# Kernel optimization log

Hardware: AMD Instinct MI355X
Metric: run time of the kernel (lower is better)

Reference implementation:

```python
import jax, jax.numpy as jnp
import numpy as np

P = 0.7
WALKS_PER_NODE = 1
WALK_LENGTH = 3


def setup_inputs() -> dict:
    key = jax.random.key(0)
    N = 1_000_000
    E = 16_000_000
    k1, k2 = jax.random.split(key)
    row = jax.random.randint(k1, (E,), 0, N)
    col = jax.random.randint(k2, (E,), 0, N)
    edge_index = jnp.stack([row, col])  # [2, E]
    return {"edge_index": edge_index, "num_nodes": N}


def reference(edge_index, num_nodes):
    E = edge_index.shape[1]
    row, col = edge_index[0], edge_index[1]

    # sort_edge_index: lexicographic sort by (row, col) via two stable argsorts
    p1 = jnp.argsort(col, stable=True)
    p2 = jnp.argsort(row[p1], stable=True)
    perm = p1[p2]
    row, col = row[perm], col[perm]

    # CSR rowptr from out-degree
    deg = jax.ops.segment_sum(jnp.ones(E, jnp.int32), row, num_segments=num_nodes)
    rowptr = jnp.concatenate([jnp.zeros(1, deg.dtype), jnp.cumsum(deg)])

    # start nodes: random permutation, take round(N*p), repeat walks_per_node times
    num_start = int(round(num_nodes * P))
    kperm, kwalk = jax.random.split(jax.random.key(42))
    start = jax.random.permutation(kperm, num_nodes)[:num_start]
    start = jnp.tile(start, WALKS_PER_NODE)  # [S]

    def step(carry, k):
        cur, active = carry
        d = deg[cur]                                  # [S] degree of current node
        act = active & (d > 0)                        # walkers with neighbors
        u = jax.random.uniform(k, cur.shape)
        off = jnp.floor(u * d.astype(u.dtype)).astype(cur.dtype)
        off = jnp.minimum(off, jnp.maximum(d - 1, 0).astype(cur.dtype))
        nxt = col[rowptr[cur] + off]                  # random neighbor gather
        # NOTE: faithful to source, e_id records current_node (used as an
        # index into the edge mask, as the original code does)
        eid = cur
        cur = jnp.where(act, nxt, cur)
        return (cur, act), (eid, act)

    keys = jax.random.split(kwalk, WALK_LENGTH)
    init = (start, jnp.ones(start.shape, bool))
    _, (e_ids, valids) = jax.lax.scan(step, init, keys)

    e_flat = e_ids.reshape(-1)
    v_flat = valids.reshape(-1)
    # scatter hits; invalid entries routed out-of-bounds and dropped
    hits = jnp.zeros(E, bool).at[jnp.where(v_flat, e_flat, E)].set(True, mode='drop')
    edge_mask = ~hits

    # fixed-shape compaction of edge_index[:, edge_mask] / edge_index[:, ~edge_mask]
    ei = jnp.stack([row, col])                        # sorted edge_index [2, E]
    order_keep = jnp.argsort(~edge_mask, stable=True)
    order_mask = jnp.argsort(edge_mask, stable=True)
    n_keep = edge_mask.sum()
    ar = jnp.arange(E)
    remaining_edges = jnp.where(ar < n_keep, ei[:, order_keep], -1)
    masked_edges = jnp.where(ar < (E - n_keep), ei[:, order_mask], -1)
    return remaining_edges, masked_edges, edge_mask
```

## Files before the change

### kernel.cpp

```cpp
#include <hip/hip_runtime.h>
#include <stdint.h>

#define THREADS 256
#define ITEMS 16
#define CHUNK (THREADS * ITEMS)
#define COLMASK 0xFFFFFu
#define EDIG 4096
#define BR 256
#define BCAP 4608
#define PDIG 1024

__host__ __device__ static inline void tf2x32(uint32_t k0, uint32_t k1,
                                              uint32_t x0, uint32_t x1,
                                              uint32_t* o0, uint32_t* o1) {
  uint32_t ks[3] = {k0, k1, k0 ^ k1 ^ 0x1BD11BDAu};
  x0 += ks[0]; x1 += ks[1];
  const uint32_t RA[4] = {13u, 15u, 26u, 6u};
  const uint32_t RB[4] = {17u, 29u, 16u, 24u};
#pragma unroll
  for (int g = 0; g < 5; ++g) {
    const uint32_t* R = (g & 1) ? RB : RA;
#pragma unroll
    for (int j = 0; j < 4; ++j) {
      x0 += x1;
      x1 = (x1 << R[j]) | (x1 >> (32u - R[j]));
      x1 ^= x0;
    }
    x0 += ks[(g + 1) % 3];
    x1 += ks[(g + 2) % 3] + (uint32_t)(g + 1);
  }
  *o0 = x0; *o1 = x1;
}

__device__ static inline uint32_t rbits32(uint32_t ka, uint32_t kb, uint32_t i) {
  uint32_t o0, o1;
  tf2x32(ka, kb, 0u, i, &o0, &o1);
  return o0 ^ o1;
}

__device__ static inline int xcd_swz(int orig, int nwg) {
  int q = nwg >> 3, r = nwg & 7;
  int xcd = orig & 7, idx = orig >> 3;
  return (xcd < r ? xcd * (q + 1) : r * (q + 1) + (xcd - r) * q) + idx;
}

__device__ static inline uint32_t block_scan_excl(uint32_t v, uint32_t* lds) {
  int t = threadIdx.x;
  lds[t] = v;
  __syncthreads();
#pragma unroll
  for (int d = 1; d < THREADS; d <<= 1) {
    uint32_t add = (t >= d) ? lds[t - d] : 0u;
    __syncthreads();
    lds[t] += add;
    __syncthreads();
  }
  return lds[t] - v;
}

__global__ void k_sums_u32(const uint32_t* __restrict__ d, int n, uint32_t* __restrict__ bsums) {
  __shared__ uint32_t lds[THREADS];
  int b = blockIdx.x, t = threadIdx.x;
  int base = b * CHUNK + t * ITEMS;
  uint32_t s = 0;
#pragma unroll
  for (int j = 0; j < ITEMS; ++j) { int i = base + j; if (i < n) s += d[i]; }
  lds[t] = s; __syncthreads();
  for (int d2 = THREADS / 2; d2 > 0; d2 >>= 1) { if (t < d2) lds[t] += lds[t + d2]; __syncthreads(); }
  if (t == 0) bsums[b] = lds[0];
}

__global__ void k_scan_single(uint32_t* __restrict__ d, int n, uint32_t* __restrict__ total_out) {
  __shared__ uint32_t lds[THREADS];
  int t = threadIdx.x;
  int K = (n + THREADS - 1) / THREADS;
  int s0 = t * K, s1 = (s0 + K < n) ? (s0 + K) : n;
  uint32_t s = 0;
  for (int j = s0; j < s1; ++j) s += d[j];
  lds[t] = s; __syncthreads();
#pragma unroll
  for (int dd = 1; dd < THREADS; dd <<= 1) {
    uint32_t a = (t >= dd) ? lds[t - dd] : 0u;
    __syncthreads();
    lds[t] += a;
    __syncthreads();
  }
  uint32_t incl = lds[t];
  if (total_out && t == THREADS - 1) *total_out = incl;
  uint32_t run = incl - s;
  for (int j = s0; j < s1; ++j) { uint32_t tmp = d[j]; d[j] = run; run += tmp; }
}

__global__ void k_excl_u32(uint32_t* __restrict__ d, int n, const uint32_t* __restrict__ bsums) {
  __shared__ uint32_t lds[THREADS];
  int b = blockIdx.x, t = threadIdx.x;
  int base = b * CHUNK + t * ITEMS;
  uint32_t v[ITEMS]; uint32_t s = 0;
#pragma unroll
  for (int j = 0; j < ITEMS; ++j) { int i = base + j; uint32_t x = (i < n) ? d[i] : 0u; v[j] = x; s += x; }
  uint32_t run = bsums[b] + block_scan_excl(s, lds);
#pragma unroll
  for (int j = 0; j < ITEMS; ++j) { int i = base + j; if (i < n) d[i] = run; run += v[j]; }
}

__global__ void k_dig_starts(const uint32_t* __restrict__ hist, int NB, int DIG, int total,
                             uint32_t* __restrict__ dstart) {
  int d = blockIdx.x * blockDim.x + threadIdx.x;
  if (d < DIG) dstart[d] = hist[(size_t)d * NB];
  else if (d == DIG) dstart[DIG] = (uint32_t)total;
}

__global__ void k_hist12(const int* __restrict__ row, int n, int NB, uint32_t* __restrict__ hist) {
  __shared__ uint32_t h[EDIG];
  int b = xcd_swz(blockIdx.x, gridDim.x), t = threadIdx.x;
#pragma unroll
  for (int g = 0; g < EDIG / THREADS; ++g) h[g * THREADS + t] = 0;
  __syncthreads();
  int base = b * CHUNK;
  for (int j = t; j < CHUNK; j += THREADS) {
    int i = base + j;
    if (i < n) atomicAdd(&h[((uint32_t)row[i]) >> 8], 1u);
  }
  __syncthreads();
#pragma unroll
  for (int g = 0; g < EDIG / THREADS; ++g) {
    int d = g * THREADS + t;
    hist[(size_t)d * NB + b] = h[d];
  }
}

__global__ __launch_bounds__(THREADS) void k_pack_scatter12(
    const int* __restrict__ row, const int* __restrict__ col,
    uint64_t* __restrict__ kout, const uint32_t* __restrict__ hist, int n, int NB) {
  constexpr int G = EDIG / THREADS;
  __shared__ uint64_t lkeys[CHUNK];
  __shared__ uint32_t cur[EDIG];
  int b = xcd_swz(blockIdx.x, gridDim.x), t = threadIdx.x;
  int base = b * CHUNK;
#pragma unroll
  for (int g = 0; g < G; ++g) cur[g * THREADS + t] = 0;
  __syncthreads();
  uint64_t mykey[ITEMS];
#pragma unroll
  for (int batch = 0; batch < ITEMS; ++batch) {
    int i = base + batch * THREADS + t;
    uint64_t key = 0ull;
    if (i < n) {
      uint32_t r = (uint32_t)row[i];
      key = ((uint64_t)r << 20) | (uint32_t)col[i];
      atomicAdd(&cur[r >> 8], 1u);
    }
    mykey[batch] = key;
  }
  __syncthreads();
  uint32_t c[G], go[G], lstv[G];
  uint32_t s = 0;
#pragma unroll
  for (int g = 0; g < G; ++g) { c[g] = cur[G * t + g]; s += c[g]; }
  uint32_t tp = block_scan_excl(s, (uint32_t*)lkeys);
  __syncthreads();
#pragma unroll
  for (int g = 0; g < G; ++g) {
    int d = G * t + g;
    go[g] = hist[(size_t)d * NB + b];
    lstv[g] = tp;
    cur[d] = tp;
    tp += c[g];
  }
  __syncthreads();
#pragma unroll
  for (int batch = 0; batch < ITEMS; ++batch) {
    int i = base + batch * THREADS + t;
    if (i < n) {
      uint64_t key = mykey[batch];
      uint32_t dig = (uint32_t)(key >> 28);
      uint32_t slot = atomicAdd(&cur[dig], 1u);
      lkeys[slot] = key;
    }
  }
  __syncthreads();
#pragma unroll
  for (int g = 0; g < G; ++g) cur[G * t + g] = go[g] - lstv[g];
  __syncthreads();
  int nloc = n - base; if (nloc > CHUNK) nloc = CHUNK;
  for (int j = t; j < nloc; j += THREADS) {
    uint64_t key = lkeys[j];
    uint32_t dig = (uint32_t)(key >> 28);
    kout[cur[dig] + (uint32_t)j] = key;
  }
}

__global__ __launch_bounds__(THREADS) void k_bucket256(
    const uint64_t* __restrict__ U0, uint64_t* __restrict__ U1,
    const uint32_t* __restrict__ dstart, int E, int Nn, int* __restrict__ rowptr) {
  __shared__ uint32_t lbuf[BCAP];
  __shared__ uint8_t  rowof[BCAP];
  __shared__ uint32_t cnt[BR];
  __shared__ uint32_t bs[BR + 1];
  int b = blockIdx.x, t = threadIdx.x;
  int s = (int)dstart[b];
  int e = (int)dstart[b + 1];
  int nseg = e - s;
  int r0 = b * BR;
  cnt[t] = 0;
  __syncthreads();
  for (int j = t; j < nseg; j += THREADS)
    atomicAdd(&cnt[(uint32_t)(U0[s + j] >> 20) & (BR - 1)], 1u);
  __syncthreads();
  uint32_t myc = cnt[t];
  uint32_t mybase = block_scan_excl(myc, lbuf);
  __syncthreads();
  bs[t] = mybase;
  if (t == THREADS - 1) bs[BR] = mybase + myc;
  cnt[t] = mybase;
  __syncthreads();
  if (nseg <= BCAP) {
    for (int j = t; j < nseg; j += THREADS) {
      uint64_t key = U0[s + j];
      uint32_t rl = (uint32_t)(key >> 20) & (BR - 1);
      uint32_t slot = atomicAdd(&cnt[rl], 1u);
      lbuf[slot] = (uint32_t)(key & COLMASK);
      rowof[slot] = (uint8_t)rl;
    }
    __syncthreads();
    for (int j = t; j < nseg; j += THREADS) {
      uint32_t key = lbuf[j];
      uint32_t rl = rowof[j];
      int a0 = (int)bs[rl], a1 = (int)bs[rl + 1];
      uint32_t rank = 0;
      for (int p = a0; p < a1; ++p) {
        uint32_t v = lbuf[p];
        rank += (v < key) || (v == key && p < j);
      }
      U1[s + a0 + (int)rank] = ((uint64_t)(uint32_t)(r0 + (int)rl) << 20) | key;
    }
  } else {
    for (int j = t; j < nseg; j += THREADS) {
      uint64_t key = U0[s + j];
      uint32_t slot = atomicAdd(&cnt[(uint32_t)(key >> 20) & (BR - 1)], 1u);
      U1[s + slot] = key;
    }
    __syncthreads();
    int a0 = s + (int)bs[t], a1 = s + (int)bs[t + 1];
    for (int a = a0 + 1; a < a1; ++a) {
      uint64_t key = U1[a];
      int p = a - 1;
      while (p >= a0 && U1[p] > key) { U1[p + 1] = U1[p]; --p; }
      U1[p + 1] = key;
    }
  }
  int r = r0 + t;
  if (r < Nn) rowptr[r] = s + (int)bs[t];
  if (b == (int)gridDim.x - 1 && t == 0) rowptr[Nn] = E;
}

__global__ void k_genkeys64(uint32_t ka, uint32_t kb, int n, uint64_t* __restrict__ K,
                            int NB, uint32_t* __restrict__ hist) {
  __shared__ uint32_t h[PDIG];
  int b = blockIdx.x, t = threadIdx.x;
#pragma unroll
  for (int g = 0; g < PDIG / THREADS; ++g) h[g * THREADS + t] = 0;
  __syncthreads();
  int base = b * CHUNK;
  for (int j = t; j < CHUNK; j += THREADS) {
    int i = base + j;
    if (i < n) {
      uint32_t rb = rbits32(ka, kb, (uint32_t)i);
      K[i] = ((uint64_t)rb << 20) | (uint32_t)i;
      atomicAdd(&h[rb >> 22], 1u);
    }
  }
  __syncthreads();
#pragma unroll
  for (int g = 0; g < PDIG / THREADS; ++g) {
    int d = g * THREADS + t;
    hist[(size_t)d * NB + b] = h[d];
  }
}

__global__ __launch_bounds__(THREADS) void k_scatter64p(
    const uint64_t* __restrict__ kin, uint64_t* __restrict__ kout,
    const uint32_t* __restrict__ hist, int n, int NB) {
  constexpr int G = PDIG / THREADS;
  __shared__ uint64_t lkeys[CHUNK];
  __shared__ uint32_t cur[PDIG];
  int b = blockIdx.x, t = threadIdx.x;
  int base = b * CHUNK;
#pragma unroll
  for (int g = 0; g < G; ++g) cur[g * THREADS + t] = 0;
  __syncthreads();
  uint64_t mykey[ITEMS];
#pragma unroll
  for (int batch = 0; batch < ITEMS; ++batch) {
    int i = base + batch * THREADS + t;
    uint64_t key = 0ull;
    if (i < n) {
      key = kin[i];
      atomicAdd(&cur[(uint32_t)(key >> 42)], 1u);
    }
    mykey[batch] = key;
  }
  __syncthreads();
  uint32_t c[G], go[G], lstv[G];
  uint32_t s = 0;
#pragma unroll
  for (int g = 0; g < G; ++g) { c[g] = cur[G * t + g]; s += c[g]; }
  uint32_t tp = block_scan_excl(s, (uint32_t*)lkeys);
  __syncthreads();
#pragma unroll
  for (int g = 0; g < G; ++g) {
    int d = G * t + g;
    go[g] = hist[(size_t)d * NB + b];
    lstv[g] = tp;
    cur[d] = tp;
    tp += c[g];
  }
  __syncthreads();
#pragma unroll
  for (int batch = 0; batch < ITEMS; ++batch) {
    int i = base + batch * THREADS + t;
    if (i < n) {
      uint64_t key = mykey[batch];
      uint32_t dig = (uint32_t)(key >> 42);
      uint32_t slot = atomicAdd(&cur[dig], 1u);
      lkeys[slot] = key;
    }
  }
  __syncthreads();
#pragma unroll
  for (int g = 0; g < G; ++g) cur[G * t + g] = go[g] - lstv[g];
  __syncthreads();
  int nloc = n - base; if (nloc > CHUNK) nloc = CHUNK;
  for (int j = t; j < nloc; j += THREADS) {
    uint64_t key = lkeys[j];
    uint32_t dig = (uint32_t)(key >> 42);
    kout[cur[dig] + (uint32_t)j] = key;
  }
}

__global__ __launch_bounds__(THREADS) void k_psort(
    const uint64_t* __restrict__ K, const uint32_t* __restrict__ dstart,
    uint32_t* __restrict__ outv, const uint32_t* __restrict__ gsrc) {
  __shared__ uint64_t sb[2048];
  int b = blockIdx.x, t = threadIdx.x;
  int s = (int)dstart[b], e = (int)dstart[b + 1];
  int nseg = e - s;
  for (int j = t; j < 2048; j += THREADS)
    sb[j] = (j < nseg) ? K[s + j] : ~0ull;
  __syncthreads();
  for (int k = 2; k <= 2048; k <<= 1) {
    for (int j = k >> 1; j > 0; j >>= 1) {
      for (int i = t; i < 2048; i += THREADS) {
        int l = i ^ j;
        if (l > i) {
          bool up = ((i & k) == 0);
          uint64_t a = sb[i], c = sb[l];
          if ((a > c) == up) { sb[i] = c; sb[l] = a; }
        }
      }
      __syncthreads();
    }
  }
  for (int j = t; j < nseg; j += THREADS) {
    uint32_t p = (uint32_t)(sb[j] & COLMASK);
    outv[s + j] = gsrc ? gsrc[p] : p;
  }
}

__global__ void k_walk(const int* __restrict__ start, int S,
                       const int* __restrict__ rowptr, const uint64_t* __restrict__ U,
                       uint8_t* __restrict__ hits,
                       uint32_t k0a, uint32_t k0b, uint32_t k1a, uint32_t k1b,
                       uint32_t k2a, uint32_t k2b) {
  int i = blockIdx.x * blockDim.x + threadIdx.x;
  int st = gridDim.x * blockDim.x;
  for (; i < S; i += st) {
    int cur = start[i];
    bool active = true;
    uint32_t ka[3] = {k0a, k1a, k2a};
    uint32_t kb[3] = {k0b, k1b, k2b};
#pragma unroll
    for (int s = 0; s < 3; ++s) {
      int rp = rowptr[cur];
      int d = rowptr[cur + 1] - rp;
      bool act = active && (d > 0);
      if (act) hits[cur] = 1;
      uint32_t bits = rbits32(ka[s], kb[s], (uint32_t)i);
      float u = __uint_as_float((bits >> 9) | 0x3f800000u) - 1.0f;
      int off = (int)floorf(u * (float)d);
      int dm1 = d - 1; if (dm1 < 0) dm1 = 0;
      if (off > dm1) off = dm1;
      if (act) cur = (int)(U[rp + off] & COLMASK);
      active = act;
    }
  }
}

__global__ void k_mask_copy(const uint8_t* __restrict__ hits, const uint64_t* __restrict__ U,
                            int Nn, uint32_t* __restrict__ bsums, uint64_t* __restrict__ hstage) {
  __shared__ uint32_t lds[THREADS];
  int b = blockIdx.x, t = threadIdx.x;
  int base = b * CHUNK + t * ITEMS;
  uint32_t s = 0;
#pragma unroll
  for (int j = 0; j < ITEMS; ++j) {
    int i = base + j;
    if (i < Nn) { s += (uint32_t)(!hits[i]); hstage[i] = U[i]; }
  }
  lds[t] = s; __syncthreads();
  for (int d2 = THREADS / 2; d2 > 0; d2 >>= 1) { if (t < d2) lds[t] += lds[t + d2]; __syncthreads(); }
  if (t == 0) bsums[b] = lds[0];
}

__global__ void k_out_tail(const uint64_t* __restrict__ U, int E, int Nn,
                           const uint32_t* __restrict__ keephead,
                           int* __restrict__ A, int* __restrict__ B, int* __restrict__ M) {
  int nm = Nn - (int)*keephead;
  int i = Nn + blockIdx.x * blockDim.x + threadIdx.x;
  int st = gridDim.x * blockDim.x;
  for (; i < E; i += st) {
    uint64_t key = U[i];
    A[i - nm] = (int)(key >> 20);
    B[i - nm] = (int)(key & COLMASK);
    M[i] = 1;
  }
}

__global__ void k_out_headCD(const uint64_t* __restrict__ hstage, const uint8_t* __restrict__ hits,
                             int Nn, const uint32_t* __restrict__ bsums,
                             int* __restrict__ A, int* __restrict__ B,
                             int* __restrict__ C, int* __restrict__ D, int* __restrict__ M) {
  __shared__ uint32_t lds[THREADS];
  int b = blockIdx.x, t = threadIdx.x;
  int base = b * CHUNK + t * ITEMS;
  uint32_t keep[ITEMS]; uint32_t s = 0;
#pragma unroll
  for (int j = 0; j < ITEMS; ++j) {
    int i = base + j;
    uint32_t k = (i < Nn) ? (uint32_t)(!hits[i]) : 0u;
    keep[j] = k; s += k;
  }
  uint32_t kr = bsums[b] + block_scan_excl(s, lds);
#pragma unroll
  for (int j = 0; j < ITEMS; ++j) {
    int i = base + j;
    if (i < Nn) {
      uint64_t key = hstage[i];
      if (keep[j]) { A[kr] = (int)(key >> 20); B[kr] = (int)(key & COLMASK); M[i] = 1; ++kr; }
      else { uint32_t mr = (uint32_t)i - kr; C[mr] = (int)(key >> 20); D[mr] = (int)(key & COLMASK); M[i] = 0; }
    }
  }
}

__global__ void k_cdfill(int E, int Nn, const uint32_t* __restrict__ keephead,
                         int* __restrict__ A, int* __restrict__ B,
                         int* __restrict__ C, int* __restrict__ D) {
  int nm = Nn - (int)*keephead;
  int j = blockIdx.x * blockDim.x + threadIdx.x;
  int st = gridDim.x * blockDim.x;
  for (; j < E; j += st) {
    if (j >= nm) { C[j] = -1; D[j] = -1; }
    if (j >= E - nm) { A[j] = -1; B[j] = -1; }
  }
}

extern "C" void kernel_launch(void* const* d_in, const int* in_sizes, int n_in,
                              void* d_out, int out_size, void* d_ws, size_t ws_size,
                              hipStream_t stream) {
  const int E = in_sizes[0] / 2;
  const int Nn = 1000000;
  const int S = 700000;
  const int NB_N = (Nn + CHUNK - 1) / CHUNK;
  const int NB_E = (E + CHUNK - 1) / CHUNK;
  const int NBUCK = (Nn + BR - 1) / BR;
  const int NB_P = (Nn + CHUNK - 1) / CHUNK;

  const int* row = (const int*)d_in[0];
  const int* col = row + (size_t)E;

  int* out = (int*)d_out;
  int* A = out;
  int* B = out + (size_t)E;
  int* C = out + (size_t)2 * E;
  int* D = out + (size_t)3 * E;
  int* M = out + (size_t)4 * E;
  uint64_t* U0 = (uint64_t*)out;
  uint64_t* U1 = (uint64_t*)(out + (size_t)2 * E);
  uint32_t* ehist = (uint32_t*)U1;

  char* w = (char*)d_ws;
  uint64_t* hstage = (uint64_t*)w;
  int* rowptr = (int*)w;
  w += (size_t)Nn * 8;
  uint8_t* hits = (uint8_t*)w; w += Nn;
  w = (char*)(((uintptr_t)w + 255) & ~(uintptr_t)255);
  uint32_t* bsums = (uint32_t*)w; w += (size_t)4096 * 4;
  uint32_t* scal = (uint32_t*)w;  w += 64;
  if ((size_t)(w - (char*)d_ws) > ws_size) return;

  uint64_t* K64a  = (uint64_t*)M;
  uint64_t* K64b  = (uint64_t*)(M + (size_t)2 * Nn);
  uint32_t* perm1 = (uint32_t*)(M + (size_t)4 * Nn);
  uint32_t* startv= (uint32_t*)(M + (size_t)5 * Nn);
  uint32_t* phist = (uint32_t*)(M + (size_t)6 * Nn);
  uint32_t* dstart= (uint32_t*)(M + (size_t)7 * Nn);

  struct KK { uint32_t a, b; };
  auto fold = [](KK k, uint32_t j) { KK r; tf2x32(k.a, k.b, 0u, j, &r.a, &r.b); return r; };
  KK base{0u, 42u};
  KK kperm = fold(base, 0u);
  KK kwalk = fold(base, 1u);
  KK keyA  = fold(kperm, 0u);
  KK sub1  = fold(kperm, 1u);
  KK sub2  = fold(keyA, 1u);
  KK wk0 = fold(kwalk, 0u), wk1 = fold(kwalk, 1u), wk2 = fold(kwalk, 2u);

  auto scan_u32 = [&](uint32_t* d, int n) {
    int SB = (n + CHUNK - 1) / CHUNK;
    k_sums_u32<<<SB, THREADS, 0, stream>>>(d, n, bsums);
    k_scan_single<<<1, THREADS, 0, stream>>>(bsums, SB, (uint32_t*)nullptr);
    k_excl_u32<<<SB, THREADS, 0, stream>>>(d, n, bsums);
  };

  hipMemsetAsync(hits, 0, (size_t)Nn, stream);

  k_hist12<<<NB_E, THREADS, 0, stream>>>(row, E, NB_E, ehist);
  scan_u32(ehist, EDIG * NB_E);
  k_dig_starts<<<(EDIG + 1 + THREADS - 1) / THREADS, THREADS, 0, stream>>>(
      ehist, NB_E, EDIG, E, dstart);
  k_pack_scatter12<<<NB_E, THREADS, 0, stream>>>(row, col, U0, ehist, E, NB_E);
  k_bucket256<<<NBUCK, THREADS, 0, stream>>>(U0, U1, dstart, E, Nn, rowptr);

  k_genkeys64<<<NB_P, THREADS, 0, stream>>>(sub1.a, sub1.b, Nn, K64a, NB_P, phist);
  scan_u32(phist, PDIG * NB_P);
  k_dig_starts<<<(PDIG + 1 + THREADS - 1) / THREADS, THREADS, 0, stream>>>(
      phist, NB_P, PDIG, Nn, dstart);
  k_scatter64p<<<NB_P, THREADS, 0, stream>>>(K64a, K64b, phist, Nn, NB_P);
  k_psort<<<PDIG, THREADS, 0, stream>>>(K64b, dstart, perm1, (const uint32_t*)nullptr);
  k_genkeys64<<<NB_P, THREADS, 0, stream>>>(sub2.a, sub2.b, Nn, K64a, NB_P, phist);
  scan_u32(phist, PDIG * NB_P);
  k_dig_starts<<<(PDIG + 1 + THREADS - 1) / THREADS, THREADS, 0, stream>>>(
      phist, NB_P, PDIG, Nn, dstart);
  k_scatter64p<<<NB_P, THREADS, 0, stream>>>(K64a, K64b, phist, Nn, NB_P);
  k_psort<<<PDIG, THREADS, 0, stream>>>(K64b, dstart, startv, perm1);

  k_walk<<<(S + THREADS - 1) / THREADS, THREADS, 0, stream>>>(
      (const int*)startv, S, rowptr, U1, hits, wk0.a, wk0.b, wk1.a, wk1.b, wk2.a, wk2.b);

  k_mask_copy<<<NB_N, THREADS, 0, stream>>>(hits, U1, Nn, bsums, hstage);
  k_scan_single<<<1, THREADS, 0, stream>>>(bsums, NB_N, &scal[0]);
  k_out_tail<<<4096, THREADS, 0, stream>>>(U1, E, Nn, &scal[0], A, B, M);
  k_out_headCD<<<NB_N, THREADS, 0, stream>>>(hstage, hits, Nn, bsums, A, B, C, D, M);
  k_cdfill<<<4096, THREADS, 0, stream>>>(E, Nn, &scal[0], A, B, C, D);
}
```

Before: 983.0 us.

## Scatter radix keys directly to global memory without shared-memory staging

```diff
diff --git a/kernel.cpp b/kernel.cpp
--- a/kernel.cpp
+++ b/kernel.cpp
@@ -132,61 +132,23 @@
 __global__ __launch_bounds__(THREADS) void k_pack_scatter12(
     const int* __restrict__ row, const int* __restrict__ col,
     uint64_t* __restrict__ kout, const uint32_t* __restrict__ hist, int n, int NB) {
-  constexpr int G = EDIG / THREADS;
-  __shared__ uint64_t lkeys[CHUNK];
   __shared__ uint32_t cur[EDIG];
   int b = xcd_swz(blockIdx.x, gridDim.x), t = threadIdx.x;
   int base = b * CHUNK;
 #pragma unroll
-  for (int g = 0; g < G; ++g) cur[g * THREADS + t] = 0;
-  __syncthreads();
-  uint64_t mykey[ITEMS];
-#pragma unroll
-  for (int batch = 0; batch < ITEMS; ++batch) {
-    int i = base + batch * THREADS + t;
-    uint64_t key = 0ull;
+  for (int g = 0; g < EDIG / THREADS; ++g) {
+    int d = g * THREADS + t;
+    cur[d] = hist[(size_t)d * NB + b];
+  }
+  __syncthreads();
+  for (int j = t; j < CHUNK; j += THREADS) {
+    int i = base + j;
     if (i < n) {
       uint32_t r = (uint32_t)row[i];
-      key = ((uint64_t)r << 20) | (uint32_t)col[i];
-      atomicAdd(&cur[r >> 8], 1u);
-    }
-    mykey[batch] = key;
-  }
-  __syncthreads();
-  uint32_t c[G], go[G], lstv[G];
-  uint32_t s = 0;
-#pragma unroll
-  for (int g = 0; g < G; ++g) { c[g] = cur[G * t + g]; s += c[g]; }
-  uint32_t tp = block_scan_excl(s, (uint32_t*)lkeys);
-  __syncthreads();
-#pragma unroll
-  for (int g = 0; g < G; ++g) {
-    int d = G * t + g;
-    go[g] = hist[(size_t)d * NB + b];
-    lstv[g] = tp;
-    cur[d] = tp;
-    tp += c[g];
-  }
-  __syncthreads();
-#pragma unroll
-  for (int batch = 0; batch < ITEMS; ++batch) {
-    int i = base + batch * THREADS + t;
-    if (i < n) {
-      uint64_t key = mykey[batch];
-      uint32_t dig = (uint32_t)(key >> 28);
-      uint32_t slot = atomicAdd(&cur[dig], 1u);
-      lkeys[slot] = key;
-    }
-  }
-  __syncthreads();
-#pragma unroll
-  for (int g = 0; g < G; ++g) cur[G * t + g] = go[g] - lstv[g];
-  __syncthreads();
-  int nloc = n - base; if (nloc > CHUNK) nloc = CHUNK;
-  for (int j = t; j < nloc; j += THREADS) {
-    uint64_t key = lkeys[j];
-    uint32_t dig = (uint32_t)(key >> 28);
-    kout[cur[dig] + (uint32_t)j] = key;
+      uint64_t key = ((uint64_t)r << 20) | (uint32_t)col[i];
+      uint32_t pos = atomicAdd(&cur[r >> 8], 1u);
+      kout[pos] = key;
+    }
   }
 }
 
@@ -194,7 +156,6 @@
     const uint64_t* __restrict__ U0, uint64_t* __restrict__ U1,
     const uint32_t* __restrict__ dstart, int E, int Nn, int* __restrict__ rowptr) {
   __shared__ uint32_t lbuf[BCAP];
-  __shared__ uint8_t  rowof[BCAP];
   __shared__ uint32_t cnt[BR];
   __shared__ uint32_t bs[BR + 1];
   int b = blockIdx.x, t = threadIdx.x;
@@ -217,22 +178,23 @@
   if (nseg <= BCAP) {
     for (int j = t; j < nseg; j += THREADS) {
       uint64_t key = U0[s + j];
-      uint32_t rl = (uint32_t)(key >> 20) & (BR - 1);
+      uint32_t klo = (uint32_t)key;
+      uint32_t rl = (klo >> 20) & (BR - 1);
       uint32_t slot = atomicAdd(&cnt[rl], 1u);
-      lbuf[slot] = (uint32_t)(key & COLMASK);
-      rowof[slot] = (uint8_t)rl;
+      lbuf[slot] = klo;
     }
     __syncthreads();
     for (int j = t; j < nseg; j += THREADS) {
-      uint32_t key = lbuf[j];
-      uint32_t rl = rowof[j];
+      uint32_t klo = lbuf[j];
+      uint32_t rl = (klo >> 20) & (BR - 1);
       int a0 = (int)bs[rl], a1 = (int)bs[rl + 1];
       uint32_t rank = 0;
       for (int p = a0; p < a1; ++p) {
         uint32_t v = lbuf[p];
-        rank += (v < key) || (v == key && p < j);
+        rank += (v < klo) || (v == klo && p < j);
       }
-      U1[s + a0 + (int)rank] = ((uint64_t)(uint32_t)(r0 + (int)rl) << 20) | key;
+      U1[s + a0 + (int)rank] =
+          ((uint64_t)(uint32_t)(r0 + (int)rl) << 20) | (klo & COLMASK);
     }
   } else {
     for (int j = t; j < nseg; j += THREADS) {
@@ -281,60 +243,22 @@
 __global__ __launch_bounds__(THREADS) void k_scatter64p(
     const uint64_t* __restrict__ kin, uint64_t* __restrict__ kout,
     const uint32_t* __restrict__ hist, int n, int NB) {
-  constexpr int G = PDIG / THREADS;
-  __shared__ uint64_t lkeys[CHUNK];
   __shared__ uint32_t cur[PDIG];
   int b = blockIdx.x, t = threadIdx.x;
   int base = b * CHUNK;
 #pragma unroll
-  for (int g = 0; g < G; ++g) cur[g * THREADS + t] = 0;
-  __syncthreads();
-  uint64_t mykey[ITEMS];
-#pragma unroll
-  for (int batch = 0; batch < ITEMS; ++batch) {
-    int i = base + batch * THREADS + t;
-    uint64_t key = 0ull;
+  for (int g = 0; g < PDIG / THREADS; ++g) {
+    int d = g * THREADS + t;
+    cur[d] = hist[(size_t)d * NB + b];
+  }
+  __syncthreads();
+  for (int j = t; j < CHUNK; j += THREADS) {
+    int i = base + j;
     if (i < n) {
-      key = kin[i];
-      atomicAdd(&cur[(uint32_t)(key >> 42)], 1u);
-    }
-    mykey[batch] = key;
-  }
-  __syncthreads();
-  uint32_t c[G], go[G], lstv[G];
-  uint32_t s = 0;
-#pragma unroll
-  for (int g = 0; g < G; ++g) { c[g] = cur[G * t + g]; s += c[g]; }
-  uint32_t tp = block_scan_excl(s, (uint32_t*)lkeys);
-  __syncthreads();
-#pragma unroll
-  for (int g = 0; g < G; ++g) {
-    int d = G * t + g;
-    go[g] = hist[(size_t)d * NB + b];
-    lstv[g] = tp;
-    cur[d] = tp;
-    tp += c[g];
-  }
-  __syncthreads();
-#pragma unroll
-  for (int batch = 0; batch < ITEMS; ++batch) {
-    int i = base + batch * THREADS + t;
-    if (i < n) {
-      uint64_t key = mykey[batch];
-      uint32_t dig = (uint32_t)(key >> 42);
-      uint32_t slot = atomicAdd(&cur[dig], 1u);
-      lkeys[slot] = key;
-    }
-  }
-  __syncthreads();
-#pragma unroll
-  for (int g = 0; g < G; ++g) cur[G * t + g] = go[g] - lstv[g];
-  __syncthreads();
-  int nloc = n - base; if (nloc > CHUNK) nloc = CHUNK;
-  for (int j = t; j < nloc; j += THREADS) {
-    uint64_t key = lkeys[j];
-    uint32_t dig = (uint32_t)(key >> 42);
-    kout[cur[dig] + (uint32_t)j] = key;
+      uint64_t key = kin[i];
+      uint32_t pos = atomicAdd(&cur[(uint32_t)(key >> 42)], 1u);
+      kout[pos] = key;
+    }
   }
 }
 
```

Result: slower. 1.157 ms (+17.7%).
